# Kernel tuning notes

Measured on AMD Instinct MI355X. Metric: run time of the kernel, lower is better.

Reference implementation:

```python
import jax, jax.numpy as jnp
import numpy as np

N = 20000      # nodes
E = 320000     # edges (avg degree 16)
IN = 512       # input feature dim
HID = 64       # hidden_dim
NH = 8         # n_heads
NC = 20        # n_classes
NG = 64        # graphs in batch
EPS = 1e-5     # batchnorm eps


def setup_inputs() -> dict:
    key = jax.random.key(0)
    ks = jax.random.split(key, 32)
    rn = lambda k, shape, s=0.05: (jax.random.normal(k, shape, jnp.float32) * s)
    inp = {
        "x": rn(ks[0], (N, IN), 1.0),
        "src": jax.random.randint(ks[1], (E,), 0, N),
        "dst": jax.random.randint(ks[2], (E,), 0, N),
        "graph_ids": jnp.sort(jax.random.randint(ks[3], (N,), 0, NG)),
        "n_graphs": NG,
        # encoder
        "W_enc": rn(ks[4], (IN, HID)), "b_enc": jnp.zeros((HID,), jnp.float32),
        # GAT layer 0
        "fc_W0": rn(ks[5], (HID, NH * HID)),
        "attn_l0": rn(ks[6], (NH, HID)), "attn_r0": rn(ks[7], (NH, HID)),
        "res_W0": rn(ks[8], (HID, NH * HID)),
        "bias0": jnp.zeros((NH * HID,), jnp.float32),
        "dp_W0": rn(ks[9], (NH * HID, HID)), "dp_b0": jnp.zeros((HID,), jnp.float32),
        # GAT layer 1
        "fc_W1": rn(ks[10], (HID, NH * HID)),
        "attn_l1": rn(ks[11], (NH, HID)), "attn_r1": rn(ks[12], (NH, HID)),
        "res_W1": rn(ks[13], (HID, NH * HID)),
        "bias1": jnp.zeros((NH * HID,), jnp.float32),
        "dp_W1": rn(ks[14], (NH * HID, HID)), "dp_b1": jnp.zeros((HID,), jnp.float32),
        # batchnorm affine
        "gamma": jnp.ones((2 * HID,), jnp.float32), "beta": jnp.zeros((2 * HID,), jnp.float32),
        # global attention pooling gate
        "gate_W": rn(ks[15], (2 * HID, 1)), "gate_b": jnp.zeros((1,), jnp.float32),
        # classifier
        "cls_W": rn(ks[16], (2 * HID, NC)), "cls_b": jnp.zeros((NC,), jnp.float32),
    }
    return inp


def gat_conv(h, fc_W, attn_l, attn_r, res_W, bias, src, dst, n_nodes):
    # DGL GATConv: fc -> per-head scalar scores -> edge softmax over incoming
    # edges -> weighted sum -> residual + bias -> leaky_relu activation.
    nh, d = attn_l.shape
    feat = (h @ fc_W).reshape(n_nodes, nh, d)              # [N,H,D]
    el = jnp.sum(feat * attn_l[None], axis=-1)             # [N,H]
    er = jnp.sum(feat * attn_r[None], axis=-1)             # [N,H]
    e = jax.nn.leaky_relu(el[src] + er[dst], 0.2)          # [E,H]
    m = jax.ops.segment_max(e, dst, num_segments=n_nodes)  # segment softmax
    ex = jnp.exp(e - m[dst])
    denom = jax.ops.segment_sum(ex, dst, num_segments=n_nodes)
    a = ex / denom[dst]                                    # [E,H]
    msg = feat[src] * a[:, :, None]                        # [E,H,D]  (dominant)
    rst = jax.ops.segment_sum(msg, dst, num_segments=n_nodes)  # [N,H,D]
    rst = rst + (h @ res_W).reshape(n_nodes, nh, d) + bias.reshape(nh, d)
    return jax.nn.leaky_relu(rst, 0.01)  # F.leaky_relu default slope


def reference(x, W_enc, b_enc,
              fc_W0, attn_l0, attn_r0, res_W0, bias0, dp_W0, dp_b0,
              fc_W1, attn_l1, attn_r1, res_W1, bias1, dp_W1, dp_b1,
              gamma, beta, gate_W, gate_b, cls_W, cls_b,
              src, dst, graph_ids, n_graphs):
    n_nodes = x.shape[0]
    he = x @ W_enc + b_enc                                  # encoder [N,HID]
    h = he
    h = gat_conv(h, fc_W0, attn_l0, attn_r0, res_W0, bias0, src, dst, n_nodes)
    h = h.reshape(n_nodes, -1) @ dp_W0 + dp_b0              # down_proj 0
    h = gat_conv(h, fc_W1, attn_l1, attn_r1, res_W1, bias1, src, dst, n_nodes)
    h = h.reshape(n_nodes, -1) @ dp_W1 + dp_b1              # down_proj 1
    hg = jnp.concatenate([h, he], axis=1)                   # [N,2*HID]
    # BatchNorm1d (training-mode batch stats, biased variance)
    mu = jnp.mean(hg, axis=0)
    var = jnp.var(hg, axis=0)
    hg = (hg - mu) * jax.lax.rsqrt(var + EPS) * gamma + beta
    # GlobalAttentionPooling: per-graph softmax over node gates
    gate = hg @ gate_W + gate_b                             # [N,1]
    gm = jax.ops.segment_max(gate, graph_ids, num_segments=n_graphs)
    ge = jnp.exp(gate - gm[graph_ids])
    gden = jax.ops.segment_sum(ge, graph_ids, num_segments=n_graphs)
    alpha = ge / gden[graph_ids]                            # [N,1]
    readout = jax.ops.segment_sum(alpha * hg, graph_ids, num_segments=n_graphs)
    return readout @ cls_W + cls_b                          # [NG,NC]
```

## Files before the change

kernel.cpp:

```cpp
#include <hip/hip_runtime.h>
#include <hip/hip_bf16.h>

#define MROWS   20000
#define N_EDGES 320000
#define DIN     512
#define HID     64
#define NH      8
#define ND      512
#define NCLS    20
#define NG      64
#define BN_EPS  1e-5f
#define PCH     16
#define BNB     256

typedef __hip_bfloat16 bf16;
typedef __attribute__((ext_vector_type(8))) short s16x8;
typedef __attribute__((ext_vector_type(4))) float f32x4;

enum { TF32 = 0, TBF16 = 1, TMODE = 2 };

__device__ __forceinline__ float ld_f32(const void* p, size_t i) { return ((const float*)p)[i]; }
__device__ __forceinline__ float ld_b16(const void* p, size_t i) { return __bfloat162float(((const bf16*)p)[i]); }

template<int T>
__device__ __forceinline__ float ldT(const void* p, size_t i, int bf) {
    if constexpr (T == TF32) return ld_f32(p, i);
    else if constexpr (T == TBF16) return ld_b16(p, i);
    else return bf ? ld_b16(p, i) : ld_f32(p, i);
}
template<int T>
__device__ __forceinline__ void stT(void* p, size_t i, int bf, float v) {
    if constexpr (T == TF32) ((float*)p)[i] = v;
    else if constexpr (T == TBF16) ((bf16*)p)[i] = __float2bfloat16(v);
    else { if (bf) ((bf16*)p)[i] = __float2bfloat16(v); else ((float*)p)[i] = v; }
}

__device__ __forceinline__ float bfbits2f(short s) {
    return __uint_as_float(((unsigned)(unsigned short)s) << 16);
}
__device__ __forceinline__ short f2bfbits(float v) {
    bf16 b = __float2bfloat16(v);
    return *reinterpret_cast<short*>(&b);
}

__global__ void detect_kernel(const void* __restrict__ gamma, int* __restrict__ mode) {
    if (threadIdx.x == 0 && blockIdx.x == 0)
        *mode = (*(const unsigned*)gamma == 0x3F800000u) ? 0 : 1;
}

struct TP { const void* src[7]; bf16* dst[7]; int K[7]; };
__global__ void transpose7_kernel(TP tp, const int* __restrict__ modep) {
    const int bf = *modep;
    int id = blockIdx.y;
    int i = blockIdx.x * 256 + threadIdx.x;
    int K = tp.K[id];
    int N = (DIN * HID) / K;
    int n = i / K, k = i - n * K;
    tp.dst[id][i] = __float2bfloat16(ldT<TMODE>(tp.src[id], (size_t)k * N + n, bf));
}

__global__ void convx_kernel(const void* __restrict__ x, bf16* __restrict__ xb,
                             const int* __restrict__ modep) {
    if (*modep) return;
    int i = (blockIdx.x * 256 + threadIdx.x) * 4;
    if (i >= MROWS * DIN) return;
    float4 v = ((const float4*)x)[i >> 2];
    xb[i + 0] = __float2bfloat16(v.x);
    xb[i + 1] = __float2bfloat16(v.y);
    xb[i + 2] = __float2bfloat16(v.z);
    xb[i + 3] = __float2bfloat16(v.w);
}

__global__ void hist_kernel(const int* __restrict__ keys, int* __restrict__ counts, int n) {
    int i = blockIdx.x * 256 + threadIdx.x;
    if (i < n) atomicAdd(&counts[keys[i]], 1);
}

__global__ void gsearch_kernel(const int* __restrict__ gids, int* __restrict__ goffs) {
    int g = threadIdx.x;
    if (g > NG) return;
    int lo = 0, hi = MROWS;
    while (lo < hi) {
        int mid = (lo + hi) >> 1;
        if (gids[mid] < g) lo = mid + 1; else hi = mid;
    }
    goffs[g] = lo;
}

__global__ __launch_bounds__(1024)
void scan1_kernel(const int* __restrict__ in, int* __restrict__ out,
                  int* __restrict__ partial, int n) {
    int i = blockIdx.x * 1024 + threadIdx.x;
    int v = (i < n) ? in[i] : 0;
    int lane = threadIdx.x & 63, wid = threadIdx.x >> 6;
    int s = v;
    #pragma unroll
    for (int o = 1; o < 64; o <<= 1) { int t = __shfl_up(s, o, 64); if (lane >= o) s += t; }
    __shared__ int wsum[16];
    if (lane == 63) wsum[wid] = s;
    __syncthreads();
    if (wid == 0 && lane < 16) {
        int t = wsum[lane];
        #pragma unroll
        for (int o = 1; o < 16; o <<= 1) { int u = __shfl_up(t, o, 64); if (lane >= o) t += u; }
        wsum[lane] = t;
    }
    __syncthreads();
    int carry = (wid > 0) ? wsum[wid - 1] : 0;
    int incl = s + carry;
    if (i < n) out[i] = incl - v;
    if (threadIdx.x == 1023) partial[blockIdx.x] = incl;
}

__global__ void scan2_kernel(int* __restrict__ partial, int nb) {
    int l = threadIdx.x;
    int v = (l < nb) ? partial[l] : 0;
    int s = v;
    #pragma unroll
    for (int o = 1; o < 64; o <<= 1) { int t = __shfl_up(s, o, 64); if (l >= o) s += t; }
    if (l < nb) partial[l] = s - v;
}

__global__ __launch_bounds__(1024)
void scan3_kernel(int* __restrict__ out, const int* __restrict__ partial, int n, int total) {
    int i = blockIdx.x * 1024 + threadIdx.x;
    if (i < n) out[i] += partial[blockIdx.x];
    if (i == 0) out[n] = total;
}

__global__ void scatter_kernel(const int* __restrict__ src, const int* __restrict__ dst,
                               const int* __restrict__ offs, int* __restrict__ cursor,
                               int* __restrict__ src_sorted) {
    int e = blockIdx.x * 256 + threadIdx.x;
    if (e < N_EDGES) {
        int d = dst[e];
        int pos = offs[d] + atomicAdd(&cursor[d], 1);
        src_sorted[pos] = src[e];
    }
}

template<int K, int NB, int NTOT>
__global__ __launch_bounds__(256)
void gemm_mfma(const void* __restrict__ Araw, const bf16* __restrict__ Aconv,
               const bf16* __restrict__ BT, const void* __restrict__ bias,
               bf16* __restrict__ C, const int* __restrict__ modep) {
    const int bf = *modep;
    const bf16* A = bf ? (const bf16*)Araw : Aconv;
    const int wid  = threadIdx.x >> 6;
    const int lane = threadIdx.x & 63;
    const int quad = lane >> 4;
    const int l16  = lane & 15;
    const int rb = blockIdx.x * 128 + wid * 32;
    const int cb = blockIdx.y * NB;
    constexpr int CT = NB / 16;
    constexpr int KC = K / 32;

    f32x4 acc[2][CT] = {};
    int r0 = rb + l16;       if (r0 >= MROWS) r0 = MROWS - 1;
    int r1 = rb + 16 + l16;  if (r1 >= MROWS) r1 = MROWS - 1;
    const bf16* a0p = A + (size_t)r0 * K + quad * 8;
    const bf16* a1p = A + (size_t)r1 * K + quad * 8;
    const bf16* btp = BT + (size_t)(cb + l16) * K + quad * 8;

    for (int kc = 0; kc < KC; ++kc) {
        s16x8 af0 = *(const s16x8*)(a0p + kc * 32);
        s16x8 af1 = *(const s16x8*)(a1p + kc * 32);
        s16x8 bfr[CT];
        #pragma unroll
        for (int ct = 0; ct < CT; ++ct)
            bfr[ct] = *(const s16x8*)(btp + (size_t)ct * 16 * K + kc * 32);
        #pragma unroll
        for (int ct = 0; ct < CT; ++ct) {
            acc[0][ct] = __builtin_amdgcn_mfma_f32_16x16x32_bf16(af0, bfr[ct], acc[0][ct], 0, 0, 0);
            acc[1][ct] = __builtin_amdgcn_mfma_f32_16x16x32_bf16(af1, bfr[ct], acc[1][ct], 0, 0, 0);
        }
    }
    #pragma unroll
    for (int ct = 0; ct < CT; ++ct) {
        int col = cb + ct * 16 + l16;
        float bb = bias ? ldT<TMODE>(bias, col, bf) : 0.f;
        #pragma unroll
        for (int rt = 0; rt < 2; ++rt) {
            #pragma unroll
            for (int rg = 0; rg < 4; ++rg) {
                int row = rb + rt * 16 + quad * 4 + rg;
                if (row < MROWS)
                    C[(size_t)row * NTOT + col] = __float2bfloat16(acc[rt][ct][rg] + bb);
            }
        }
    }
}

__global__ __launch_bounds__(256)
void gemm_fcres(const bf16* __restrict__ A, const bf16* __restrict__ BT_fc,
                const bf16* __restrict__ BT_res, const void* __restrict__ bias,
                const void* __restrict__ attn_l, const void* __restrict__ attn_r,
                bf16* __restrict__ feat, bf16* __restrict__ rst,
                float* __restrict__ el, float* __restrict__ er,
                const int* __restrict__ modep) {
    const int bf = *modep;
    const bool isres = blockIdx.y >= 4;
    const int yy = blockIdx.y & 3;
    const bf16* BT = isres ? BT_res : BT_fc;
    bf16* C = isres ? rst : feat;
    const int wid  = threadIdx.x >> 6;
    const int lane = threadIdx.x & 63;
    const int quad = lane >> 4;
    const int l16  = lane & 15;
    const int rb = blockIdx.x * 128 + wid * 32;
    const int cb = yy * 128;
    constexpr int CT = 8;
    constexpr int K  = HID;
    constexpr int KC = K / 32;

    f32x4 acc[2][CT] = {};
    int r0 = rb + l16;       if (r0 >= MROWS) r0 = MROWS - 1;
    int r1 = rb + 16 + l16;  if (r1 >= MROWS) r1 = MROWS - 1;
    const bf16* a0p = A + (size_t)r0 * K + quad * 8;
    const bf16* a1p = A + (size_t)r1 * K + quad * 8;
    const bf16* btp = BT + (size_t)(cb + l16) * K + quad * 8;

    #pragma unroll
    for (int kc = 0; kc < KC; ++kc) {
        s16x8 af0 = *(const s16x8*)(a0p + kc * 32);
        s16x8 af1 = *(const s16x8*)(a1p + kc * 32);
        s16x8 bfr[CT];
        #pragma unroll
        for (int ct = 0; ct < CT; ++ct)
            bfr[ct] = *(const s16x8*)(btp + (size_t)ct * 16 * K + kc * 32);
        #pragma unroll
        for (int ct = 0; ct < CT; ++ct) {
            acc[0][ct] = __builtin_amdgcn_mfma_f32_16x16x32_bf16(af0, bfr[ct], acc[0][ct], 0, 0, 0);
            acc[1][ct] = __builtin_amdgcn_mfma_f32_16x16x32_bf16(af1, bfr[ct], acc[1][ct], 0, 0, 0);
        }
    }
    #pragma unroll
    for (int ct = 0; ct < CT; ++ct) {
        int col = cb + ct * 16 + l16;
        float bb = isres ? ldT<TMODE>(bias, col, bf) : 0.f;
        #pragma unroll
        for (int rt = 0; rt < 2; ++rt) {
            #pragma unroll
            for (int rg = 0; rg < 4; ++rg) {
                int row = rb + rt * 16 + quad * 4 + rg;
                if (row < MROWS)
                    C[(size_t)row * ND + col] = __float2bfloat16(acc[rt][ct][rg] + bb);
            }
        }
    }
    if (!isres) {
        float al[CT], ar[CT];
        #pragma unroll
        for (int ct = 0; ct < CT; ++ct) {
            int col = cb + ct * 16 + l16;
            al[ct] = ldT<TMODE>(attn_l, col, bf);
            ar[ct] = ldT<TMODE>(attn_r, col, bf);
        }
        #pragma unroll
        for (int rt = 0; rt < 2; ++rt) {
            #pragma unroll
            for (int rg = 0; rg < 4; ++rg) {
                float e0 = 0.f, e1 = 0.f, f0 = 0.f, f1 = 0.f;
                #pragma unroll
                for (int ct = 0; ct < 4; ++ct) {
                    e0 += acc[rt][ct][rg] * al[ct];
                    f0 += acc[rt][ct][rg] * ar[ct];
                    e1 += acc[rt][ct + 4][rg] * al[ct + 4];
                    f1 += acc[rt][ct + 4][rg] * ar[ct + 4];
                }
                #pragma unroll
                for (int o = 1; o < 16; o <<= 1) {
                    e0 += __shfl_xor(e0, o, 64);
                    e1 += __shfl_xor(e1, o, 64);
                    f0 += __shfl_xor(f0, o, 64);
                    f1 += __shfl_xor(f1, o, 64);
                }
                int row = rb + rt * 16 + quad * 4 + rg;
                if (row < MROWS) {
                    if (l16 == 0) { el[row * 8 + 2 * yy] = e0;     er[row * 8 + 2 * yy] = f0; }
                    if (l16 == 1) { el[row * 8 + 2 * yy + 1] = e1; er[row * 8 + 2 * yy + 1] = f1; }
                }
            }
        }
    }
}

__global__ __launch_bounds__(256)
void agg_kernel(const bf16* __restrict__ feat, const float* __restrict__ el,
                const float* __restrict__ er, const int* __restrict__ offs,
                const int* __restrict__ srcs, bf16* __restrict__ rst) {
    int gid = blockIdx.x * 256 + threadIdx.x;
    int n = gid >> 6;
    int l = threadIdx.x & 63;
    if (n >= MROWS) return;
    int hh = l >> 3;
    int e0 = offs[n], e1 = offs[n + 1];
    float er_h = er[n * 8 + hh];
    float acc[8] = {0.f, 0.f, 0.f, 0.f, 0.f, 0.f, 0.f, 0.f};
    float den = 0.f;
    for (int base = e0; base < e1; base += 64) {
        int cnt = min(64, e1 - base);
        int sv = (base + l < e1) ? srcs[base + l] : 0;
        for (int e = 0; e < cnt; ++e) {
            int s = __shfl(sv, e, 64);
            float sc = el[s * 8 + hh] + er_h;
            sc = sc > 0.f ? sc : 0.2f * sc;
            float w = __expf(fminf(sc, 30.f));
            s16x8 f8 = *(const s16x8*)(feat + (size_t)s * ND + l * 8);
            den += w;
            #pragma unroll
            for (int j = 0; j < 8; ++j)
                acc[j] += bfbits2f(f8[j]) * w;
        }
    }
    float inv = (den > 0.f) ? 1.f / den : 0.f;
    s16x8* rp = (s16x8*)(rst + (size_t)n * ND + l * 8);
    s16x8 rr = *rp;
    s16x8 ro;
    #pragma unroll
    for (int j = 0; j < 8; ++j) {
        float r = bfbits2f(rr[j]) + acc[j] * inv;
        r = r > 0.f ? r : 0.01f * r;
        ro[j] = f2bfbits(r);
    }
    *rp = ro;
}

__global__ void bn_part_kernel(const bf16* __restrict__ h2, const bf16* __restrict__ he,
                               float* __restrict__ psum, float* __restrict__ psq) {
    int t = threadIdx.x;
    int b = blockIdx.x;
    int beg = (int)((long)MROWS * b / BNB);
    int end = (int)((long)MROWS * (b + 1) / BNB);
    const bf16* srcb = (t < 64) ? h2 : he;
    int col = t & 63;
    float s = 0.f, s2 = 0.f;
    for (int r = beg; r < end; ++r) {
        float v = __bfloat162float(srcb[(size_t)r * 64 + col]);
        s += v;
        s2 += v * v;
    }
    psum[b * 128 + t] = s;
    psq[b * 128 + t] = s2;
}

__global__ void bn_reduce_kernel(const float* __restrict__ psum, const float* __restrict__ psq,
                                 const void* __restrict__ gamma, const void* __restrict__ beta,
                                 float* __restrict__ scale, float* __restrict__ shift,
                                 const int* __restrict__ modep) {
    const int bf = *modep;
    int t = threadIdx.x;
    float s = 0.f, s2 = 0.f;
    for (int b = 0; b < BNB; ++b) { s += psum[b * 128 + t]; s2 += psq[b * 128 + t]; }
    float mu = s * (1.f / MROWS);
    float var = s2 * (1.f / MROWS) - mu * mu;
    float inv = rsqrtf(fmaxf(var, 0.f) + BN_EPS);
    float a = ldT<TMODE>(gamma, t, bf) * inv;
    scale[t] = a;
    shift[t] = ldT<TMODE>(beta, t, bf) - mu * a;
}

__global__ __launch_bounds__(256)
void gate_kernel(const bf16* __restrict__ h2, const bf16* __restrict__ he,
                 const float* __restrict__ scale, const float* __restrict__ shift,
                 const void* __restrict__ gate_W, const void* __restrict__ gate_b,
                 float* __restrict__ ge, const int* __restrict__ modep) {
    const int bf = *modep;
    int gid = blockIdx.x * 256 + threadIdx.x;
    int r = gid >> 6;
    int l = threadIdx.x & 63;
    if (r >= MROWS) return;
    float v0 = __bfloat162float(h2[(size_t)r * 64 + l]) * scale[l] + shift[l];
    float v1 = __bfloat162float(he[(size_t)r * 64 + l]) * scale[64 + l] + shift[64 + l];
    float s = v0 * ldT<TMODE>(gate_W, l, bf) + v1 * ldT<TMODE>(gate_W, 64 + l, bf);
    #pragma unroll
    for (int o = 32; o > 0; o >>= 1) s += __shfl_xor(s, o, 64);
    if (l == 0) {
        float g = s + ldT<TMODE>(gate_b, 0, bf);
        ge[r] = __expf(fminf(fmaxf(g, -60.f), 30.f));
    }
}

__global__ void pool1_kernel(const bf16* __restrict__ h2, const bf16* __restrict__ he,
                             const float* __restrict__ scale, const float* __restrict__ shift,
                             const float* __restrict__ ge, const int* __restrict__ goffs,
                             float* __restrict__ pacc, float* __restrict__ pden) {
    int g = blockIdx.x;
    int c = blockIdx.y;
    int t = threadIdx.x;
    int r0 = goffs[g], r1 = goffs[g + 1];
    int len = r1 - r0;
    int beg = r0 + (int)((long)len * c / PCH);
    int end = r0 + (int)((long)len * (c + 1) / PCH);
    const bf16* srcb = (t < 64) ? h2 : he;
    int col = t & 63;
    float sc = scale[t], sh = shift[t];
    float acc = 0.f, den = 0.f;
    for (int r = beg; r < end; ++r) {
        float wg = ge[r];
        float v = __bfloat162float(srcb[(size_t)r * 64 + col]) * sc + sh;
        den += wg;
        acc += wg * v;
    }
    pacc[((size_t)g * PCH + c) * 128 + t] = acc;
    if (t == 0) pden[g * PCH + c] = den;
}

__global__ void pool2_kernel(const float* __restrict__ pacc, const float* __restrict__ pden,
                             float* __restrict__ readout) {
    int g = blockIdx.x;
    int t = threadIdx.x;
    float acc = 0.f, den = 0.f;
    #pragma unroll
    for (int c = 0; c < PCH; ++c) {
        acc += pacc[((size_t)g * PCH + c) * 128 + t];
        den += pden[g * PCH + c];
    }
    readout[g * 128 + t] = (den > 0.f) ? acc / den : 0.f;
}

__global__ void cls_kernel(const float* __restrict__ readout, const void* __restrict__ W,
                           const void* __restrict__ b, void* __restrict__ out,
                           const int* __restrict__ modep) {
    const int bf = *modep;
    int i = blockIdx.x * 256 + threadIdx.x;
    if (i >= NG * NCLS) return;
    int g = i / NCLS, c = i - g * NCLS;
    float acc = ldT<TMODE>(b, c, bf);
    #pragma unroll 8
    for (int k = 0; k < 128; ++k)
        acc += readout[g * 128 + k] * ldT<TMODE>(W, k * NCLS + c, bf);
    stT<TMODE>(out, i, bf, acc);
}

extern "C" void kernel_launch(void* const* d_in, const int* in_sizes, int n_in,
                              void* d_out, int out_size, void* d_ws, size_t ws_size,
                              hipStream_t stream) {
    const void* x       = d_in[0];
    const int*  src     = (const int*)d_in[1];
    const int*  dst     = (const int*)d_in[2];
    const int*  gids    = (const int*)d_in[3];
    const void* W_enc   = d_in[5];
    const void* b_enc   = d_in[6];
    const void* fc_W0   = d_in[7];
    const void* attn_l0 = d_in[8];
    const void* attn_r0 = d_in[9];
    const void* res_W0  = d_in[10];
    const void* bias0   = d_in[11];
    const void* dp_W0   = d_in[12];
    const void* dp_b0   = d_in[13];
    const void* fc_W1   = d_in[14];
    const void* attn_l1 = d_in[15];
    const void* attn_r1 = d_in[16];
    const void* res_W1  = d_in[17];
    const void* bias1   = d_in[18];
    const void* dp_W1   = d_in[19];
    const void* dp_b1   = d_in[20];
    const void* gamma   = d_in[21];
    const void* beta    = d_in[22];
    const void* gate_W  = d_in[23];
    const void* gate_b  = d_in[24];
    const void* cls_W   = d_in[25];
    const void* cls_b   = d_in[26];

    char* wsc = (char*)d_ws;
    size_t off = 0;
    auto alloc = [&](size_t bytes) -> void* {
        void* p = wsc + off;
        off = (off + bytes + 255) & ~(size_t)255;
        return p;
    };
    bf16*  he        = (bf16*) alloc((size_t)MROWS * HID * 2);
    bf16*  h         = (bf16*) alloc((size_t)MROWS * HID * 2);
    bf16*  h2        = (bf16*) alloc((size_t)MROWS * HID * 2);
    bf16*  feat      = (bf16*) alloc((size_t)MROWS * ND * 2);
    bf16*  rst       = (bf16*) alloc((size_t)MROWS * ND * 2);
    bf16*  xb        = rst;
    bf16*  bt_enc    = (bf16*) alloc((size_t)DIN * HID * 2);
    bf16*  bt_fc0    = (bf16*) alloc((size_t)HID * ND * 2);
    bf16*  bt_res0   = (bf16*) alloc((size_t)HID * ND * 2);
    bf16*  bt_dp0    = (bf16*) alloc((size_t)ND * HID * 2);
    bf16*  bt_fc1    = (bf16*) alloc((size_t)HID * ND * 2);
    bf16*  bt_res1   = (bf16*) alloc((size_t)HID * ND * 2);
    bf16*  bt_dp1    = (bf16*) alloc((size_t)ND * HID * 2);
    float* el        = (float*)alloc((size_t)MROWS * 8 * 4);
    float* er        = (float*)alloc((size_t)MROWS * 8 * 4);
    float* ge        = (float*)alloc((size_t)MROWS * 4);
    float* readout   = (float*)alloc((size_t)NG * 128 * 4);
    int*   src_sorted= (int*)  alloc((size_t)N_EDGES * 4);
    int*   offs      = (int*)  alloc((size_t)(MROWS + 1) * 4);
    int*   goffs     = (int*)  alloc((size_t)(NG + 1) * 4);
    int*   spartial  = (int*)  alloc(64 * 4);
    float* psum      = (float*)alloc((size_t)BNB * 128 * 4);
    float* psq       = (float*)alloc((size_t)BNB * 128 * 4);
    float* pacc      = (float*)alloc((size_t)NG * PCH * 128 * 4);
    float* pden      = (float*)alloc((size_t)NG * PCH * 4);
    float* bnscale   = (float*)alloc(128 * 4);
    float* bnshift   = (float*)alloc(128 * 4);
    int*   mode      = (int*)  alloc(4);
    size_t zbytes = (size_t)MROWS * 4 * 2;
    char*  zbase  = (char*)alloc(zbytes);
    int* counts  = (int*)zbase;
    int* cursor  = counts + MROWS;

    hipMemsetAsync(zbase, 0, zbytes, stream);
    detect_kernel<<<1, 64, 0, stream>>>(gamma, mode);

    TP tp;
    tp.src[0] = W_enc;  tp.K[0] = DIN;
    tp.src[1] = fc_W0;  tp.K[1] = HID;
    tp.src[2] = res_W0; tp.K[2] = HID;
    tp.src[3] = dp_W0;  tp.K[3] = ND;
    tp.src[4] = fc_W1;  tp.K[4] = HID;
    tp.src[5] = res_W1; tp.K[5] = HID;
    tp.src[6] = dp_W1;  tp.K[6] = ND;
    tp.dst[0] = bt_enc; tp.dst[1] = bt_fc0; tp.dst[2] = bt_res0; tp.dst[3] = bt_dp0;
    tp.dst[4] = bt_fc1; tp.dst[5] = bt_res1; tp.dst[6] = bt_dp1;
    transpose7_kernel<<<dim3((DIN * HID) / 256, 7), 256, 0, stream>>>(tp, mode);
    convx_kernel<<<(MROWS * DIN / 4 + 255) / 256, 256, 0, stream>>>(x, xb, mode);

    hist_kernel<<<(N_EDGES + 255) / 256, 256, 0, stream>>>(dst, counts, N_EDGES);
    gsearch_kernel<<<1, 128, 0, stream>>>(gids, goffs);
    const int SB = (MROWS + 1023) / 1024;
    scan1_kernel<<<SB, 1024, 0, stream>>>(counts, offs, spartial, MROWS);
    scan2_kernel<<<1, 64, 0, stream>>>(spartial, SB);
    scan3_kernel<<<SB, 1024, 0, stream>>>(offs, spartial, MROWS, N_EDGES);
    scatter_kernel<<<(N_EDGES + 255) / 256, 256, 0, stream>>>(src, dst, offs, cursor, src_sorted);

    const int GX = (MROWS + 127) / 128;

    gemm_mfma<DIN, 64, 64><<<dim3(GX, 1), 256, 0, stream>>>(x, xb, bt_enc, b_enc, he, mode);

    gemm_fcres<<<dim3(GX, 8), 256, 0, stream>>>(he, bt_fc0, bt_res0, bias0, attn_l0, attn_r0,
                                                feat, rst, el, er, mode);
    agg_kernel<<<(MROWS * 64) / 256, 256, 0, stream>>>(feat, el, er, offs, src_sorted, rst);
    gemm_mfma<ND, 64, 64><<<dim3(GX, 1), 256, 0, stream>>>(rst, rst, bt_dp0, dp_b0, h, mode);

    gemm_fcres<<<dim3(GX, 8), 256, 0, stream>>>(h, bt_fc1, bt_res1, bias1, attn_l1, attn_r1,
                                                feat, rst, el, er, mode);
    agg_kernel<<<(MROWS * 64) / 256, 256, 0, stream>>>(feat, el, er, offs, src_sorted, rst);
    gemm_mfma<ND, 64, 64><<<dim3(GX, 1), 256, 0, stream>>>(rst, rst, bt_dp1, dp_b1, h2, mode);

    bn_part_kernel<<<BNB, 128, 0, stream>>>(h2, he, psum, psq);
    bn_reduce_kernel<<<1, 128, 0, stream>>>(psum, psq, gamma, beta, bnscale, bnshift, mode);
    gate_kernel<<<(MROWS * 64 + 255) / 256, 256, 0, stream>>>(h2, he, bnscale, bnshift, gate_W, gate_b, ge, mode);
    pool1_kernel<<<dim3(NG, PCH), 128, 0, stream>>>(h2, he, bnscale, bnshift, ge, goffs, pacc, pden);
    pool2_kernel<<<NG, 128, 0, stream>>>(pacc, pden, readout);
    cls_kernel<<<(NG * NCLS + 255) / 256, 256, 0, stream>>>(readout, cls_W, cls_b, d_out, mode);
}
```

Before: 479.2 us.

## Cut launches, batch edge gathers in aggregation, and inline dtype detection

Removes the mode-detect kernel and has each kernel read gamma directly to choose the dtype path. Replaces the three-kernel scan with a single-block scan and fuses pool2 with the classifier. Makes the x conversion a grid-stride loop. In the GAT aggregation it computes edge weights for 8 edges in parallel and issues 8 independent row gathers before accumulating, which raises memory-level parallelism. The trade-offs are a serialized single-block scan and extra shuffles in the aggregation.

```diff
diff --git a/kernel.cpp b/kernel.cpp
--- a/kernel.cpp
+++ b/kernel.cpp
@@ -19,6 +19,10 @@
 
 enum { TF32 = 0, TBF16 = 1, TMODE = 2 };
 
+__device__ __forceinline__ int getmode(const void* gamma) {
+    return *(const unsigned*)gamma != 0x3F800000u;
+}
+
 __device__ __forceinline__ float ld_f32(const void* p, size_t i) { return ((const float*)p)[i]; }
 __device__ __forceinline__ float ld_b16(const void* p, size_t i) { return __bfloat162float(((const bf16*)p)[i]); }
 
@@ -43,14 +47,9 @@
     return *reinterpret_cast<short*>(&b);
 }
 
-__global__ void detect_kernel(const void* __restrict__ gamma, int* __restrict__ mode) {
-    if (threadIdx.x == 0 && blockIdx.x == 0)
-        *mode = (*(const unsigned*)gamma == 0x3F800000u) ? 0 : 1;
-}
-
 struct TP { const void* src[7]; bf16* dst[7]; int K[7]; };
-__global__ void transpose7_kernel(TP tp, const int* __restrict__ modep) {
-    const int bf = *modep;
+__global__ void transpose7_kernel(TP tp, const void* __restrict__ gamma) {
+    const int bf = getmode(gamma);
     int id = blockIdx.y;
     int i = blockIdx.x * 256 + threadIdx.x;
     int K = tp.K[id];
@@ -60,15 +59,17 @@
 }
 
 __global__ void convx_kernel(const void* __restrict__ x, bf16* __restrict__ xb,
-                             const int* __restrict__ modep) {
-    if (*modep) return;
-    int i = (blockIdx.x * 256 + threadIdx.x) * 4;
-    if (i >= MROWS * DIN) return;
-    float4 v = ((const float4*)x)[i >> 2];
-    xb[i + 0] = __float2bfloat16(v.x);
-    xb[i + 1] = __float2bfloat16(v.y);
-    xb[i + 2] = __float2bfloat16(v.z);
-    xb[i + 3] = __float2bfloat16(v.w);
+                             const void* __restrict__ gamma) {
+    if (getmode(gamma)) return;
+    const int total4 = MROWS * DIN / 4;
+    for (int i4 = blockIdx.x * 256 + threadIdx.x; i4 < total4; i4 += gridDim.x * 256) {
+        float4 v = ((const float4*)x)[i4];
+        int i = i4 * 4;
+        xb[i + 0] = __float2bfloat16(v.x);
+        xb[i + 1] = __float2bfloat16(v.y);
+        xb[i + 2] = __float2bfloat16(v.z);
+        xb[i + 3] = __float2bfloat16(v.w);
+    }
 }
 
 __global__ void hist_kernel(const int* __restrict__ keys, int* __restrict__ counts, int n) {
@@ -88,44 +89,31 @@
 }
 
 __global__ __launch_bounds__(1024)
-void scan1_kernel(const int* __restrict__ in, int* __restrict__ out,
-                  int* __restrict__ partial, int n) {
-    int i = blockIdx.x * 1024 + threadIdx.x;
-    int v = (i < n) ? in[i] : 0;
-    int lane = threadIdx.x & 63, wid = threadIdx.x >> 6;
-    int s = v;
-    #pragma unroll
-    for (int o = 1; o < 64; o <<= 1) { int t = __shfl_up(s, o, 64); if (lane >= o) s += t; }
+void scan_kernel(const int* __restrict__ in, int* __restrict__ out) {
+    const int C = 20;
+    int t = threadIdx.x;
+    int beg = t * C; if (beg > MROWS) beg = MROWS;
+    int end = beg + C; if (end > MROWS) end = MROWS;
+    int s = 0;
+    for (int i = beg; i < end; ++i) s += in[i];
+    int lane = t & 63, wid = t >> 6;
+    int ps = s;
+    #pragma unroll
+    for (int o = 1; o < 64; o <<= 1) { int u = __shfl_up(ps, o, 64); if (lane >= o) ps += u; }
     __shared__ int wsum[16];
-    if (lane == 63) wsum[wid] = s;
+    if (lane == 63) wsum[wid] = ps;
     __syncthreads();
     if (wid == 0 && lane < 16) {
-        int t = wsum[lane];
-        #pragma unroll
-        for (int o = 1; o < 16; o <<= 1) { int u = __shfl_up(t, o, 64); if (lane >= o) t += u; }
-        wsum[lane] = t;
+        int u = wsum[lane];
+        #pragma unroll
+        for (int o = 1; o < 16; o <<= 1) { int v = __shfl_up(u, o, 64); if (lane >= o) u += v; }
+        wsum[lane] = u;
     }
     __syncthreads();
-    int carry = (wid > 0) ? wsum[wid - 1] : 0;
-    int incl = s + carry;
-    if (i < n) out[i] = incl - v;
-    if (threadIdx.x == 1023) partial[blockIdx.x] = incl;
-}
-
-__global__ void scan2_kernel(int* __restrict__ partial, int nb) {
-    int l = threadIdx.x;
-    int v = (l < nb) ? partial[l] : 0;
-    int s = v;
-    #pragma unroll
-    for (int o = 1; o < 64; o <<= 1) { int t = __shfl_up(s, o, 64); if (l >= o) s += t; }
-    if (l < nb) partial[l] = s - v;
-}
-
-__global__ __launch_bounds__(1024)
-void scan3_kernel(int* __restrict__ out, const int* __restrict__ partial, int n, int total) {
-    int i = blockIdx.x * 1024 + threadIdx.x;
-    if (i < n) out[i] += partial[blockIdx.x];
-    if (i == 0) out[n] = total;
+    int carry = ps - s + (wid > 0 ? wsum[wid - 1] : 0);
+    int run = carry;
+    for (int i = beg; i < end; ++i) { out[i] = run; run += in[i]; }
+    if (t == 0) out[MROWS] = N_EDGES;
 }
 
 __global__ void scatter_kernel(const int* __restrict__ src, const int* __restrict__ dst,
@@ -143,8 +131,8 @@
 __global__ __launch_bounds__(256)
 void gemm_mfma(const void* __restrict__ Araw, const bf16* __restrict__ Aconv,
                const bf16* __restrict__ BT, const void* __restrict__ bias,
-               bf16* __restrict__ C, const int* __restrict__ modep) {
-    const int bf = *modep;
+               bf16* __restrict__ C, const void* __restrict__ gamma) {
+    const int bf = getmode(gamma);
     const bf16* A = bf ? (const bf16*)Araw : Aconv;
     const int wid  = threadIdx.x >> 6;
     const int lane = threadIdx.x & 63;
@@ -197,8 +185,8 @@
                 const void* __restrict__ attn_l, const void* __restrict__ attn_r,
                 bf16* __restrict__ feat, bf16* __restrict__ rst,
                 float* __restrict__ el, float* __restrict__ er,
-                const int* __restrict__ modep) {
-    const int bf = *modep;
+                const void* __restrict__ gamma) {
+    const int bf = getmode(gamma);
     const bool isres = blockIdx.y >= 4;
     const int yy = blockIdx.y & 3;
     const bf16* BT = isres ? BT_res : BT_fc;
@@ -294,23 +282,46 @@
     int l = threadIdx.x & 63;
     if (n >= MROWS) return;
     int hh = l >> 3;
+    int hw = l & 7;
     int e0 = offs[n], e1 = offs[n + 1];
-    float er_h = er[n * 8 + hh];
+    float er_w = er[n * 8 + hw];
     float acc[8] = {0.f, 0.f, 0.f, 0.f, 0.f, 0.f, 0.f, 0.f};
     float den = 0.f;
-    for (int base = e0; base < e1; base += 64) {
-        int cnt = min(64, e1 - base);
-        int sv = (base + l < e1) ? srcs[base + l] : 0;
-        for (int e = 0; e < cnt; ++e) {
-            int s = __shfl(sv, e, 64);
-            float sc = el[s * 8 + hh] + er_h;
-            sc = sc > 0.f ? sc : 0.2f * sc;
-            float w = __expf(fminf(sc, 30.f));
-            s16x8 f8 = *(const s16x8*)(feat + (size_t)s * ND + l * 8);
-            den += w;
+    const bf16* fcol = feat + l * 8;
+
+    for (int base = e0; base < e1; base += 8) {
+        int m = e1 - base; if (m > 8) m = 8;
+        int sv = (base + hw < e1) ? srcs[base + hw] : 0;
+        int sj = __shfl(sv, l >> 3, 64);
+        float sc = el[sj * 8 + hw] + er_w;
+        sc = sc > 0.f ? sc : 0.2f * sc;
+        float w = ((l >> 3) < m) ? __expf(fminf(sc, 30.f)) : 0.f;
+        if (m == 8) {
+            s16x8 rows[8];
+            float ws[8];
             #pragma unroll
-            for (int j = 0; j < 8; ++j)
-                acc[j] += bfbits2f(f8[j]) * w;
+            for (int j = 0; j < 8; ++j) {
+                int s = __shfl(sv, j, 64);
+                rows[j] = *(const s16x8*)(fcol + (size_t)s * ND);
+                ws[j] = __shfl(w, (j << 3) | hh, 64);
+            }
+            #pragma unroll
+            for (int j = 0; j < 8; ++j) {
+                den += ws[j];
+                #pragma unroll
+                for (int k = 0; k < 8; ++k)
+                    acc[k] += bfbits2f(rows[j][k]) * ws[j];
+            }
+        } else {
+            for (int j = 0; j < m; ++j) {
+                int s = __shfl(sv, j, 64);
+                float wj = __shfl(w, (j << 3) | hh, 64);
+                s16x8 f8 = *(const s16x8*)(fcol + (size_t)s * ND);
+                den += wj;
+                #pragma unroll
+                for (int k = 0; k < 8; ++k)
+                    acc[k] += bfbits2f(f8[k]) * wj;
+            }
         }
     }
     float inv = (den > 0.f) ? 1.f / den : 0.f;
@@ -346,9 +357,8 @@
 
 __global__ void bn_reduce_kernel(const float* __restrict__ psum, const float* __restrict__ psq,
                                  const void* __restrict__ gamma, const void* __restrict__ beta,
-                                 float* __restrict__ scale, float* __restrict__ shift,
-                                 const int* __restrict__ modep) {
-    const int bf = *modep;
+                                 float* __restrict__ scale, float* __restrict__ shift) {
+    const int bf = getmode(gamma);
     int t = threadIdx.x;
     float s = 0.f, s2 = 0.f;
     for (int b = 0; b < BNB; ++b) { s += psum[b * 128 + t]; s2 += psq[b * 128 + t]; }
@@ -364,8 +374,8 @@
 void gate_kernel(const bf16* __restrict__ h2, const bf16* __restrict__ he,
                  const float* __restrict__ scale, const float* __restrict__ shift,
                  const void* __restrict__ gate_W, const void* __restrict__ gate_b,
-                 float* __restrict__ ge, const int* __restrict__ modep) {
-    const int bf = *modep;
+                 float* __restrict__ ge, const void* __restrict__ gamma) {
+    const int bf = getmode(gamma);
     int gid = blockIdx.x * 256 + threadIdx.x;
     int r = gid >> 6;
     int l = threadIdx.x & 63;
@@ -406,8 +416,10 @@
     if (t == 0) pden[g * PCH + c] = den;
 }
 
-__global__ void pool2_kernel(const float* __restrict__ pacc, const float* __restrict__ pden,
-                             float* __restrict__ readout) {
+__global__ void pool2cls_kernel(const float* __restrict__ pacc, const float* __restrict__ pden,
+                                const void* __restrict__ W, const void* __restrict__ b,
+                                void* __restrict__ out, const void* __restrict__ gamma) {
+    const int bf = getmode(gamma);
     int g = blockIdx.x;
     int t = threadIdx.x;
     float acc = 0.f, den = 0.f;
@@ -416,21 +428,16 @@
         acc += pacc[((size_t)g * PCH + c) * 128 + t];
         den += pden[g * PCH + c];
     }
-    readout[g * 128 + t] = (den > 0.f) ? acc / den : 0.f;
-}
-
-__global__ void cls_kernel(const float* __restrict__ readout, const void* __restrict__ W,
-                           const void* __restrict__ b, void* __restrict__ out,
-                           const int* __restrict__ modep) {
-    const int bf = *modep;
-    int i = blockIdx.x * 256 + threadIdx.x;
-    if (i >= NG * NCLS) return;
-    int g = i / NCLS, c = i - g * NCLS;
-    float acc = ldT<TMODE>(b, c, bf);
-    #pragma unroll 8
-    for (int k = 0; k < 128; ++k)
-        acc += readout[g * 128 + k] * ldT<TMODE>(W, k * NCLS + c, bf);
-    stT<TMODE>(out, i, bf, acc);
+    __shared__ float ro[128];
+    ro[t] = (den > 0.f) ? acc / den : 0.f;
+    __syncthreads();
+    if (t < NCLS) {
+        float s = ldT<TMODE>(b, t, bf);
+        #pragma unroll 8
+        for (int k = 0; k < 128; ++k)
+            s += ro[k] * ldT<TMODE>(W, k * NCLS + t, bf);
+        stT<TMODE>(out, g * NCLS + t, bf, s);
+    }
 }
 
 extern "C" void kernel_launch(void* const* d_in, const int* in_sizes, int n_in,
@@ -486,25 +493,21 @@
     float* el        = (float*)alloc((size_t)MROWS * 8 * 4);
     float* er        = (float*)alloc((size_t)MROWS * 8 * 4);
     float* ge        = (float*)alloc((size_t)MROWS * 4);
-    float* readout   = (float*)alloc((size_t)NG * 128 * 4);
     int*   src_sorted= (int*)  alloc((size_t)N_EDGES * 4);
     int*   offs      = (int*)  alloc((size_t)(MROWS + 1) * 4);
     int*   goffs     = (int*)  alloc((size_t)(NG + 1) * 4);
-    int*   spartial  = (int*)  alloc(64 * 4);
     float* psum      = (float*)alloc((size_t)BNB * 128 * 4);
     float* psq       = (float*)alloc((size_t)BNB * 128 * 4);
     float* pacc      = (float*)alloc((size_t)NG * PCH * 128 * 4);
     float* pden      = (float*)alloc((size_t)NG * PCH * 4);
     float* bnscale   = (float*)alloc(128 * 4);
     float* bnshift   = (float*)alloc(128 * 4);
-    int*   mode      = (int*)  alloc(4);
     size_t zbytes = (size_t)MROWS * 4 * 2;
     char*  zbase  = (char*)alloc(zbytes);
     int* counts  = (int*)zbase;
     int* cursor  = counts + MROWS;
 
     hipMemsetAsync(zbase, 0, zbytes, stream);
-    detect_kernel<<<1, 64, 0, stream>>>(gamma, mode);
 
     TP tp;
     tp.src[0] = W_enc;  tp.K[0] = DIN;
@@ -516,35 +519,31 @@
     tp.src[6] = dp_W1;  tp.K[6] = ND;
     tp.dst[0] = bt_enc; tp.dst[1] = bt_fc0; tp.dst[2] = bt_res0; tp.dst[3] = bt_dp0;
     tp.dst[4] = bt_fc1; tp.dst[5] = bt_res1; tp.dst[6] = bt_dp1;
-    transpose7_kernel<<<dim3((DIN * HID) / 256, 7), 256, 0, stream>>>(tp, mode);
-    convx_kernel<<<(MROWS * DIN / 4 + 255) / 256, 256, 0, stream>>>(x, xb, mode);
+    transpose7_kernel<<<dim3((DIN * HID) / 256, 7), 256, 0, stream>>>(tp, gamma);
+    convx_kernel<<<640, 256, 0, stream>>>(x, xb, gamma);
 
     hist_kernel<<<(N_EDGES + 255) / 256, 256, 0, stream>>>(dst, counts, N_EDGES);
     gsearch_kernel<<<1, 128, 0, stream>>>(gids, goffs);
-    const int SB = (MROWS + 1023) / 1024;
-    scan1_kernel<<<SB, 1024, 0, stream>>>(counts, offs, spartial, MROWS);
-    scan2_kernel<<<1, 64, 0, stream>>>(spartial, SB);
-    scan3_kernel<<<SB, 1024, 0, stream>>>(offs, spartial, MROWS, N_EDGES);
+    scan_kernel<<<1, 1024, 0, stream>>>(counts, offs);
     scatter_kernel<<<(N_EDGES + 255) / 256, 256, 0, stream>>>(src, dst, offs, cursor, src_sorted);
 
     const int GX = (MROWS + 127) / 128;
 
-    gemm_mfma<DIN, 64, 64><<<dim3(GX, 1), 256, 0, stream>>>(x, xb, bt_enc, b_enc, he, mode);
+    gemm_mfma<DIN, 64, 64><<<dim3(GX, 1), 256, 0, stream>>>(x, xb, bt_enc, b_enc, he, gamma);
 
     gemm_fcres<<<dim3(GX, 8), 256, 0, stream>>>(he, bt_fc0, bt_res0, bias0, attn_l0, attn_r0,
-                                                feat, rst, el, er, mode);
+                                                feat, rst, el, er, gamma);
     agg_kernel<<<(MROWS * 64) / 256, 256, 0, stream>>>(feat, el, er, offs, src_sorted, rst);
-    gemm_mfma<ND, 64, 64><<<dim3(GX, 1), 256, 0, stream>>>(rst, rst, bt_dp0, dp_b0, h, mode);
+    gemm_mfma<ND, 64, 64><<<dim3(GX, 1), 256, 0, stream>>>(rst, rst, bt_dp0, dp_b0, h, gamma);
 
     gemm_fcres<<<dim3(GX, 8), 256, 0, stream>>>(h, bt_fc1, bt_res1, bias1, attn_l1, attn_r1,
-                                                feat, rst, el, er, mode);
+                                                feat, rst, el, er, gamma);
     agg_kernel<<<(MROWS * 64) / 256, 256, 0, stream>>>(feat, el, er, offs, src_sorted, rst);
-    gemm_mfma<ND, 64, 64><<<dim3(GX, 1), 256, 0, stream>>>(rst, rst, bt_dp1, dp_b1, h2, mode);
+    gemm_mfma<ND, 64, 64><<<dim3(GX, 1), 256, 0, stream>>>(rst, rst, bt_dp1, dp_b1, h2, gamma);
 
     bn_part_kernel<<<BNB, 128, 0, stream>>>(h2, he, psum, psq);
-    bn_reduce_kernel<<<1, 128, 0, stream>>>(psum, psq, gamma, beta, bnscale, bnshift, mode);
-    gate_kernel<<<(MROWS * 64 + 255) / 256, 256, 0, stream>>>(h2, he, bnscale, bnshift, gate_W, gate_b, ge, mode);
+    bn_reduce_kernel<<<1, 128, 0, stream>>>(psum, psq, gamma, beta, bnscale, bnshift);
+    gate_kernel<<<(MROWS * 64 + 255) / 256, 256, 0, stream>>>(h2, he, bnscale, bnshift, gate_W, gate_b, ge, gamma);
     pool1_kernel<<<dim3(NG, PCH), 128, 0, stream>>>(h2, he, bnscale, bnshift, ge, goffs, pacc, pden);
-    pool2_kernel<<<NG, 128, 0, stream>>>(pacc, pden, readout);
-    cls_kernel<<<(NG * NCLS + 255) / 256, 256, 0, stream>>>(readout, cls_W, cls_b, d_out, mode);
-}
+    pool2cls_kernel<<<NG, 128, 0, stream>>>(pacc, pden, cls_W, cls_b, d_out, gamma);
+}
```

Result: no change. 487.5 us (+1.7%).
